# Kernel optimization log

Measured on AMD Instinct MI355X. Metric: run time of the kernel, lower is better.

The kernel has to match this reference:

```python
import jax, jax.numpy as jnp
import numpy as np

B, C, N, M, K = 1, 64, 65536, 65536, 16
H, O = 64, 128  # mlp hidden, out_channels


def setup_inputs() -> dict:
    key = jax.random.key(0)
    ks = jax.random.split(key, 8)
    return {
        "x": jax.random.normal(ks[0], (B, C, N), dtype=jnp.float32),
        "pos": jax.random.normal(ks[1], (B, 3, N), dtype=jnp.float32),
        "support_points": jax.random.normal(ks[2], (B, 3, M), dtype=jnp.float32),
        "W1": jax.random.normal(ks[3], (H, C + 3), dtype=jnp.float32) * 0.05,
        "b1": jax.random.normal(ks[4], (H,), dtype=jnp.float32) * 0.05,
        "W2": jax.random.normal(ks[5], (O, H), dtype=jnp.float32) * 0.05,
        "b2": jax.random.normal(ks[6], (O,), dtype=jnp.float32) * 0.05,
        "indices": jax.random.randint(ks[7], (B, M, K), 0, N, dtype=jnp.int64),
    }


def _gather_points(t, indices):
    # t: [B, C, N], indices: [B, M, K] -> [B, C, M, K]
    b, c, n = t.shape
    m, k = indices.shape[1], indices.shape[2]
    idx = indices.reshape(b, 1, m * k)  # broadcasts over channel dim
    return jnp.take_along_axis(t, idx, axis=2).reshape(b, c, m, k)


def reference(x, pos, support_points, W1, b1, W2, b2, indices):
    # gather neighbor features and positions: [B, C, M, K], [B, 3, M, K]
    feats = _gather_points(x, indices)
    pts = _gather_points(pos, indices) - support_points[:, :, :, None]
    h = jnp.concatenate([feats, pts], axis=1)  # [B, C+3, M, K]
    # shared per-point MLP (1x1 Conv2d == channel contraction)
    h = jnp.einsum("oc,bcmk->bomk", W1, h) + b1[None, :, None, None]
    h = jax.nn.relu(h)
    h = jnp.einsum("oc,bcmk->bomk", W2, h) + b2[None, :, None, None]
    # max-pool over neighborhood K -> [B, O, M]
    return jnp.max(h, axis=3)
```

## Files before the change

### kernel.cpp

```cpp
#include <hip/hip_runtime.h>

#define NPTS 65536
#define MPTS 65536
#define FSTR 88

typedef __attribute__((ext_vector_type(8))) short bf16x8;
typedef __attribute__((ext_vector_type(4))) float f32x4;

__device__ __forceinline__ float bflo(unsigned int u){ union{unsigned int i; float f;} v; v.i = u<<16; return v.f; }
__device__ __forceinline__ float bfhi(unsigned int u){ union{unsigned int i; float f;} v; v.i = u & 0xffff0000u; return v.f; }
__device__ __forceinline__ unsigned short f2bf(float f){
  union{float f; unsigned int i;} v; v.f=f;
  unsigned int r = v.i + 0x7fffu + ((v.i>>16)&1u);
  return (unsigned short)(r>>16);
}

__global__ __launch_bounds__(256) void pack_all(
    const float* __restrict__ x, const float* __restrict__ pos,
    const float* __restrict__ W1, const float* __restrict__ W2,
    unsigned short* __restrict__ P2,
    unsigned short* __restrict__ W1F, unsigned short* __restrict__ W2F) {
  __shared__ unsigned int tile[64 * 37];
  const int t = threadIdx.x;
  const int n0 = blockIdx.x * 64;
  const int p = t & 63, cq = t >> 6;
  const int n = n0 + p;
  #pragma unroll
  for (int jj = 0; jj < 8; ++jj) {
    const int c = cq * 16 + 2 * jj;
    const unsigned int lo = f2bf(x[(size_t)c * NPTS + n]);
    const unsigned int hi = f2bf(x[(size_t)(c + 1) * NPTS + n]);
    tile[p * 37 + cq * 8 + jj] = lo | (hi << 16);
  }
  if (cq == 0) {
    const unsigned int a = f2bf(pos[n]);
    const unsigned int b = f2bf(pos[NPTS + n]);
    const unsigned int cc = f2bf(pos[2 * NPTS + n]);
    tile[p * 37 + 32] = a | (b << 16);
    tile[p * 37 + 33] = cc;
    tile[p * 37 + 34] = 0u;
    tile[p * 37 + 35] = 0u;
  }
  __syncthreads();
  unsigned int* Pd = (unsigned int*)(P2 + (size_t)n0 * 72);
  #pragma unroll
  for (int i = 0; i < 9; ++i) {
    const int u = t + i * 256;
    const int nl = u / 36, d = u - nl * 36;
    Pd[u] = tile[nl * 37 + d];
  }
  if (blockIdx.x < 7) {
    const int f = blockIdx.x * 256 + t;
    if (f < 768) {
      const int kt = f >> 8, rem = f & 255, nt = rem >> 6, lane = rem & 63;
      const int h = nt*16 + (lane & 15);
      const int c0 = kt*32 + (lane >> 4) * 8;
      #pragma unroll
      for (int j = 0; j < 8; ++j) {
        const int c = c0 + j;
        W1F[f*8 + j] = (c < 67) ? f2bf(W1[h*67 + c]) : (unsigned short)0;
      }
    } else if (f < 1792) {
      const int g = f - 768;
      const int kt = g >> 9, rem = g & 511, ot = rem >> 6, lane = rem & 63;
      const int o = ot*16 + (lane & 15);
      const int h0 = kt*32 + (lane >> 4) * 8;
      #pragma unroll
      for (int j = 0; j < 8; ++j) W2F[g*8 + j] = f2bf(W2[o*64 + h0 + j]);
    }
  }
}

#define MFMA16(a,b,c) __builtin_amdgcn_mfma_f32_16x16x32_bf16((a),(b),(c),0,0,0)

__global__ __launch_bounds__(256, 3) void pointnet_mfma(
    const unsigned short* __restrict__ P2,
    const float* __restrict__ sup,
    const unsigned short* __restrict__ W1F,
    const float* __restrict__ b1,
    const unsigned short* __restrict__ W2F,
    const float* __restrict__ b2,
    const int* __restrict__ indices,
    float* __restrict__ out) {
  __shared__ __align__(16) char smem[53248];
  unsigned short* featB = (unsigned short*)smem;
  unsigned short* hlds  = (unsigned short*)smem;
  float* smax = (float*)(smem + 45056);

  const int t = threadIdx.x;
  const int m0 = blockIdx.x * 16;
  const int lane = t & 63, w = t >> 6, quad = lane >> 4, lr = lane & 15;

  {
    const int idx = indices[m0*16 + t];
    const uint4* src = (const uint4*)(P2 + (size_t)idx * 72);
    uint4 u[9];
    #pragma unroll
    for (int i = 0; i < 9; ++i) u[i] = src[i];
    const int mm = m0 + (t >> 4);
    const float s0 = sup[mm], s1 = sup[MPTS + mm], s2 = sup[2*MPTS + mm];
    const float p0 = bflo(u[8].x), p1 = bfhi(u[8].x), p2 = bflo(u[8].y);
    u[8].x = (unsigned int)f2bf(p0 - s0) | ((unsigned int)f2bf(p1 - s1) << 16);
    u[8].y = (unsigned int)f2bf(p2 - s2);
    u[8].z = 0u; u[8].w = 0u;
    uint4* dst = (uint4*)(featB + t * FSTR);
    #pragma unroll
    for (int i = 0; i < 9; ++i) dst[i] = u[i];
  }

  bf16x8 w1f[3][4];
  #pragma unroll
  for (int kt = 0; kt < 3; ++kt)
    #pragma unroll
    for (int nt = 0; nt < 4; ++nt)
      w1f[kt][nt] = ((const bf16x8*)W1F)[(kt*4 + nt)*64 + lane];
  float b1s[4];
  #pragma unroll
  for (int nt = 0; nt < 4; ++nt) b1s[nt] = b1[nt*16 + lr];

  const f32x4 fz = {0.f, 0.f, 0.f, 0.f};
  f32x4 acc[4][4];
  #pragma unroll
  for (int pt = 0; pt < 4; ++pt)
    #pragma unroll
    for (int nt = 0; nt < 4; ++nt) acc[pt][nt] = fz;
  #pragma unroll
  for (int kt = 0; kt < 2; ++kt) {
    bf16x8 af[4];
    #pragma unroll
    for (int pt = 0; pt < 4; ++pt)
      af[pt] = *(const bf16x8*)&featB[(w*64 + pt*16 + lr)*FSTR + kt*32 + quad*8];
    #pragma unroll
    for (int pt = 0; pt < 4; ++pt)
      #pragma unroll
      for (int nt = 0; nt < 4; ++nt)
        acc[pt][nt] = MFMA16(af[pt], w1f[kt][nt], acc[pt][nt]);
  }
  {
    const bf16x8 zv = {0,0,0,0,0,0,0,0};
    bf16x8 af[4];
    #pragma unroll
    for (int pt = 0; pt < 4; ++pt) {
      const bf16x8 v = *(const bf16x8*)&featB[(w*64 + pt*16 + lr)*FSTR + 64];
      af[pt] = (quad == 0) ? v : zv;
    }
    #pragma unroll
    for (int pt = 0; pt < 4; ++pt)
      #pragma unroll
      for (int nt = 0; nt < 4; ++nt)
        acc[pt][nt] = MFMA16(af[pt], w1f[2][nt], acc[pt][nt]);
  }

  #pragma unroll
  for (int pt = 0; pt < 4; ++pt)
    #pragma unroll
    for (int nt = 0; nt < 4; ++nt) {
      const int h = nt*16 + lr;
      const int pbase = w*64 + pt*16 + quad*4;
      #pragma unroll
      for (int r = 0; r < 4; ++r)
        hlds[(pbase + r)*FSTR + h] = f2bf(fmaxf(acc[pt][nt][r] + b1s[nt], 0.f));
    }

  #pragma unroll
  for (int oh = 0; oh < 2; ++oh) {
    bf16x8 w2f[2][4];
    #pragma unroll
    for (int kt = 0; kt < 2; ++kt)
      #pragma unroll
      for (int ot = 0; ot < 4; ++ot)
        w2f[kt][ot] = ((const bf16x8*)W2F)[(kt*8 + oh*4 + ot)*64 + lane];
    f32x4 a2[4][4];
    #pragma unroll
    for (int pt = 0; pt < 4; ++pt)
      #pragma unroll
      for (int ot = 0; ot < 4; ++ot) a2[pt][ot] = fz;
    #pragma unroll
    for (int kt = 0; kt < 2; ++kt) {
      bf16x8 ah[4];
      #pragma unroll
      for (int pt = 0; pt < 4; ++pt)
        ah[pt] = *(const bf16x8*)&hlds[(w*64 + pt*16 + lr)*FSTR + kt*32 + quad*8];
      #pragma unroll
      for (int pt = 0; pt < 4; ++pt)
        #pragma unroll
        for (int ot = 0; ot < 4; ++ot)
          a2[pt][ot] = MFMA16(ah[pt], w2f[kt][ot], a2[pt][ot]);
    }
    #pragma unroll
    for (int pt = 0; pt < 4; ++pt)
      #pragma unroll
      for (int ot = 0; ot < 4; ++ot) {
        f32x4 v4 = a2[pt][ot];
        float v = fmaxf(fmaxf(v4[0], v4[1]), fmaxf(v4[2], v4[3]));
        v = fmaxf(v, __shfl_xor(v, 16));
        v = fmaxf(v, __shfl_xor(v, 32));
        if (quad == 0) smax[(w*4 + pt)*128 + oh*64 + ot*16 + lr] = v;
      }
  }
  __syncthreads();

  #pragma unroll
  for (int i = 0; i < 2; ++i) {
    const int u = t + i*256;
    const int o = u >> 2, mg = u & 3;
    const float bb = b2[o];
    float4 val;
    val.x = smax[(mg*4 + 0)*128 + o] + bb;
    val.y = smax[(mg*4 + 1)*128 + o] + bb;
    val.z = smax[(mg*4 + 2)*128 + o] + bb;
    val.w = smax[(mg*4 + 3)*128 + o] + bb;
    *(float4*)(out + (size_t)o * MPTS + m0 + mg*4) = val;
  }
}

__global__ __launch_bounds__(256) void pointnet_fallback(
    const float* __restrict__ x, const float* __restrict__ pos,
    const float* __restrict__ sup,
    const float* __restrict__ W1, const float* __restrict__ b1,
    const float* __restrict__ W2, const float* __restrict__ b2,
    const int* __restrict__ indices, float* __restrict__ out) {
  __shared__ float sfeat[16][68];
  __shared__ float shid[16][64];
  __shared__ float smax[4][128];
  __shared__ int sidx[16];
  const int t = threadIdx.x;
  const int m = blockIdx.x;
  if (t < 16) sidx[t] = indices[m*16 + t];
  const float sup0 = sup[m], sup1 = sup[MPTS + m], sup2 = sup[2*MPTS + m];
  __syncthreads();
  for (int u = t; u < 16*17; u += 256) {
    const int k = u / 17, c4 = (u - k*17) * 4;
    const int idx = sidx[k];
    float4 w;
    if (c4 < 64) {
      w.x = x[(size_t)(c4+0)*NPTS + idx]; w.y = x[(size_t)(c4+1)*NPTS + idx];
      w.z = x[(size_t)(c4+2)*NPTS + idx]; w.w = x[(size_t)(c4+3)*NPTS + idx];
    } else {
      w.x = pos[idx] - sup0; w.y = pos[NPTS + idx] - sup1;
      w.z = pos[2*NPTS + idx] - sup2; w.w = 0.f;
    }
    *(float4*)&sfeat[k][c4] = w;
  }
  const int h = t & 63, kg = t >> 6;
  float w1r[68];
  #pragma unroll
  for (int c = 0; c < 67; ++c) w1r[c] = W1[h*67 + c];
  w1r[67] = 0.f;
  const float bias1 = b1[h];
  __syncthreads();
  #pragma unroll
  for (int j = 0; j < 4; ++j) {
    const int k = kg*4 + j;
    float a = bias1;
    const float4* rr = (const float4*)sfeat[k];
    #pragma unroll
    for (int q = 0; q < 17; ++q) {
      const float4 v = rr[q];
      a += w1r[q*4+0]*v.x + w1r[q*4+1]*v.y + w1r[q*4+2]*v.z + w1r[q*4+3]*v.w;
    }
    shid[k][h] = fmaxf(a, 0.f);
  }
  const int ow = t & 63;
  float w2a[64], w2b[64];
  #pragma unroll
  for (int hh = 0; hh < 64; ++hh) { w2a[hh] = W2[ow*64 + hh]; w2b[hh] = W2[(ow+64)*64 + hh]; }
  __syncthreads();
  float mxa = -3.0e38f, mxb = -3.0e38f;
  #pragma unroll
  for (int j = 0; j < 4; ++j) {
    const int k = kg*4 + j;
    const float4* hr = (const float4*)shid[k];
    float pa = 0.f, pb = 0.f;
    #pragma unroll
    for (int q = 0; q < 16; ++q) {
      const float4 v = hr[q];
      pa += w2a[q*4+0]*v.x + w2a[q*4+1]*v.y + w2a[q*4+2]*v.z + w2a[q*4+3]*v.w;
      pb += w2b[q*4+0]*v.x + w2b[q*4+1]*v.y + w2b[q*4+2]*v.z + w2b[q*4+3]*v.w;
    }
    mxa = fmaxf(mxa, pa); mxb = fmaxf(mxb, pb);
  }
  smax[kg][ow] = mxa; smax[kg][64 + ow] = mxb;
  __syncthreads();
  if (t < 128) {
    out[(size_t)t * MPTS + m] =
        fmaxf(fmaxf(smax[0][t], smax[1][t]), fmaxf(smax[2][t], smax[3][t])) + b2[t];
  }
}

extern "C" void kernel_launch(void* const* d_in, const int* in_sizes, int n_in,
                              void* d_out, int out_size, void* d_ws, size_t ws_size,
                              hipStream_t stream) {
  const float* x   = (const float*)d_in[0];
  const float* pos = (const float*)d_in[1];
  const float* sup = (const float*)d_in[2];
  const float* W1  = (const float*)d_in[3];
  const float* b1  = (const float*)d_in[4];
  const float* W2  = (const float*)d_in[5];
  const float* b2  = (const float*)d_in[6];
  const int* indices = (const int*)d_in[7];
  float* out = (float*)d_out;

  const size_t P2_BYTES  = (size_t)NPTS * 72 * 2;
  const size_t W1F_BYTES = 768 * 8 * 2;
  const size_t W2F_BYTES = 1024 * 8 * 2;
  if (ws_size >= P2_BYTES + W1F_BYTES + W2F_BYTES) {
    unsigned short* P2  = (unsigned short*)d_ws;
    unsigned short* W1F = (unsigned short*)((char*)d_ws + P2_BYTES);
    unsigned short* W2F = (unsigned short*)((char*)d_ws + P2_BYTES + W1F_BYTES);
    pack_all<<<NPTS/64, 256, 0, stream>>>(x, pos, W1, W2, P2, W1F, W2F);
    pointnet_mfma<<<MPTS/16, 256, 0, stream>>>(P2, sup, W1F, b1, W2F, b2, indices, out);
  } else {
    pointnet_fallback<<<MPTS, 256, 0, stream>>>(x, pos, sup, W1, b1, W2, b2, indices, out);
  }
}
```

Before: 153.3 us.

## Keep hidden layer in registers via transposed MFMA, drop LDS round-trip and smax

```diff
diff --git a/kernel.cpp b/kernel.cpp
--- a/kernel.cpp
+++ b/kernel.cpp
@@ -2,7 +2,7 @@
 
 #define NPTS 65536
 #define MPTS 65536
-#define FSTR 88
+#define FSTR 72
 
 typedef __attribute__((ext_vector_type(8))) short bf16x8;
 typedef __attribute__((ext_vector_type(4))) float f32x4;
@@ -15,11 +15,14 @@
   return (unsigned short)(r>>16);
 }
 
+#define MFMA32(a,b,c) __builtin_amdgcn_mfma_f32_16x16x32_bf16((a),(b),(c),0,0,0)
+
 __global__ __launch_bounds__(256) void pack_all(
     const float* __restrict__ x, const float* __restrict__ pos,
     const float* __restrict__ W1, const float* __restrict__ W2,
     unsigned short* __restrict__ P2,
-    unsigned short* __restrict__ W1F, unsigned short* __restrict__ W2F) {
+    unsigned short* __restrict__ W1F,
+    unsigned short* __restrict__ W2F) {
   __shared__ unsigned int tile[64 * 37];
   const int t = threadIdx.x;
   const int n0 = blockIdx.x * 64;
@@ -42,38 +45,42 @@
     tile[p * 37 + 35] = 0u;
   }
   __syncthreads();
-  unsigned int* Pd = (unsigned int*)(P2 + (size_t)n0 * 72);
+  unsigned int* Pd = (unsigned int*)(P2 + (size_t)n0 * FSTR);
   #pragma unroll
   for (int i = 0; i < 9; ++i) {
     const int u = t + i * 256;
     const int nl = u / 36, d = u - nl * 36;
     Pd[u] = tile[nl * 37 + d];
   }
-  if (blockIdx.x < 7) {
-    const int f = blockIdx.x * 256 + t;
-    if (f < 768) {
-      const int kt = f >> 8, rem = f & 255, nt = rem >> 6, lane = rem & 63;
-      const int h = nt*16 + (lane & 15);
-      const int c0 = kt*32 + (lane >> 4) * 8;
+  const int wid = blockIdx.x * 256 + t;
+  if (wid < 768) {
+    const int f = wid >> 6, lane = wid & 63;
+    const int q = lane >> 4, lr = lane & 15;
+    if (f < 8) {
+      const int kt = f >> 2, nt = f & 3;
+      #pragma unroll
+      for (int j = 0; j < 8; ++j)
+        W1F[wid*8 + j] = f2bf(W1[(nt*16 + lr)*67 + kt*32 + q*8 + j]);
+    } else {
+      const int nt = f - 8;
       #pragma unroll
       for (int j = 0; j < 8; ++j) {
-        const int c = c0 + j;
-        W1F[f*8 + j] = (c < 67) ? f2bf(W1[h*67 + c]) : (unsigned short)0;
+        const int c = 64 + q*4 + j;
+        W1F[wid*8 + j] = (j < 4 && c < 67) ? f2bf(W1[(nt*16 + lr)*67 + c]) : (unsigned short)0;
       }
-    } else if (f < 1792) {
-      const int g = f - 768;
-      const int kt = g >> 9, rem = g & 511, ot = rem >> 6, lane = rem & 63;
-      const int o = ot*16 + (lane & 15);
-      const int h0 = kt*32 + (lane >> 4) * 8;
-      #pragma unroll
-      for (int j = 0; j < 8; ++j) W2F[g*8 + j] = f2bf(W2[o*64 + h0 + j]);
-    }
-  }
-}
-
-#define MFMA16(a,b,c) __builtin_amdgcn_mfma_f32_16x16x32_bf16((a),(b),(c),0,0,0)
-
-__global__ __launch_bounds__(256, 3) void pointnet_mfma(
+    }
+  } else if (wid < 768 + 2048) {
+    const int gg = wid - 768;
+    const int g = gg >> 6, lane = gg & 63;
+    const int q = lane >> 4, lr = lane & 15;
+    const int nt = g >> 3, ot = g & 7;
+    #pragma unroll
+    for (int j = 0; j < 8; ++j)
+      W2F[gg*8 + j] = (j < 4) ? f2bf(W2[(ot*16 + lr)*64 + nt*16 + q*4 + j]) : (unsigned short)0;
+  }
+}
+
+__global__ __launch_bounds__(256, 4) void pointnet_mfma(
     const unsigned short* __restrict__ P2,
     const float* __restrict__ sup,
     const unsigned short* __restrict__ W1F,
@@ -82,10 +89,7 @@
     const float* __restrict__ b2,
     const int* __restrict__ indices,
     float* __restrict__ out) {
-  __shared__ __align__(16) char smem[53248];
-  unsigned short* featB = (unsigned short*)smem;
-  unsigned short* hlds  = (unsigned short*)smem;
-  float* smax = (float*)(smem + 45056);
+  __shared__ __align__(16) unsigned short featB[256 * FSTR];
 
   const int t = threadIdx.x;
   const int m0 = blockIdx.x * 16;
@@ -93,7 +97,7 @@
 
   {
     const int idx = indices[m0*16 + t];
-    const uint4* src = (const uint4*)(P2 + (size_t)idx * 72);
+    const uint4* src = (const uint4*)(P2 + (size_t)idx * FSTR);
     uint4 u[9];
     #pragma unroll
     for (int i = 0; i < 9; ++i) u[i] = src[i];
@@ -108,109 +112,92 @@
     for (int i = 0; i < 9; ++i) dst[i] = u[i];
   }
 
-  bf16x8 w1f[3][4];
-  #pragma unroll
-  for (int kt = 0; kt < 3; ++kt)
+  const f32x4 fz = {0.f, 0.f, 0.f, 0.f};
+  f32x4 acc1[4][4];
+  #pragma unroll
+  for (int nt = 0; nt < 4; ++nt)
+    #pragma unroll
+    for (int pt = 0; pt < 4; ++pt) acc1[nt][pt] = fz;
+
+  #pragma unroll
+  for (int kt = 0; kt < 2; ++kt) {
+    bf16x8 wa[4];
     #pragma unroll
     for (int nt = 0; nt < 4; ++nt)
-      w1f[kt][nt] = ((const bf16x8*)W1F)[(kt*4 + nt)*64 + lane];
-  float b1s[4];
-  #pragma unroll
-  for (int nt = 0; nt < 4; ++nt) b1s[nt] = b1[nt*16 + lr];
-
-  const f32x4 fz = {0.f, 0.f, 0.f, 0.f};
-  f32x4 acc[4][4];
-  #pragma unroll
-  for (int pt = 0; pt < 4; ++pt)
-    #pragma unroll
-    for (int nt = 0; nt < 4; ++nt) acc[pt][nt] = fz;
-  #pragma unroll
-  for (int kt = 0; kt < 2; ++kt) {
-    bf16x8 af[4];
+      wa[nt] = ((const bf16x8*)W1F)[(kt*4 + nt)*64 + lane];
+    bf16x8 bf[4];
     #pragma unroll
     for (int pt = 0; pt < 4; ++pt)
-      af[pt] = *(const bf16x8*)&featB[(w*64 + pt*16 + lr)*FSTR + kt*32 + quad*8];
-    #pragma unroll
-    for (int pt = 0; pt < 4; ++pt)
-      #pragma unroll
-      for (int nt = 0; nt < 4; ++nt)
-        acc[pt][nt] = MFMA16(af[pt], w1f[kt][nt], acc[pt][nt]);
+      bf[pt] = *(const bf16x8*)&featB[(w*64 + pt*16 + lr)*FSTR + kt*32 + quad*8];
+    #pragma unroll
+    for (int nt = 0; nt < 4; ++nt)
+      #pragma unroll
+      for (int pt = 0; pt < 4; ++pt)
+        acc1[nt][pt] = MFMA32(wa[nt], bf[pt], acc1[nt][pt]);
   }
   {
-    const bf16x8 zv = {0,0,0,0,0,0,0,0};
-    bf16x8 af[4];
+    bf16x8 wa16[4];
+    #pragma unroll
+    for (int nt = 0; nt < 4; ++nt)
+      wa16[nt] = ((const bf16x8*)W1F)[(8 + nt)*64 + lane];
+    bf16x8 bt[4];
     #pragma unroll
     for (int pt = 0; pt < 4; ++pt) {
-      const bf16x8 v = *(const bf16x8*)&featB[(w*64 + pt*16 + lr)*FSTR + 64];
-      af[pt] = (quad == 0) ? v : zv;
-    }
-    #pragma unroll
-    for (int pt = 0; pt < 4; ++pt)
-      #pragma unroll
-      for (int nt = 0; nt < 4; ++nt)
-        acc[pt][nt] = MFMA16(af[pt], w1f[2][nt], acc[pt][nt]);
-  }
-
-  #pragma unroll
-  for (int pt = 0; pt < 4; ++pt)
+      const uint2 d = *(const uint2*)&featB[(w*64 + pt*16 + lr)*FSTR + 64 + (quad & 1)*4];
+      union { unsigned int u[4]; bf16x8 v; } mk;
+      mk.u[0] = d.x; mk.u[1] = d.y; mk.u[2] = 0u; mk.u[3] = 0u;
+      bt[pt] = mk.v;
+    }
+    #pragma unroll
+    for (int nt = 0; nt < 4; ++nt)
+      #pragma unroll
+      for (int pt = 0; pt < 4; ++pt)
+        acc1[nt][pt] = MFMA32(wa16[nt], bt[pt], acc1[nt][pt]);
+  }
+
+  unsigned int dwpk[4][4][2];
+  #pragma unroll
+  for (int nt = 0; nt < 4; ++nt) {
+    const float4 bb = *(const float4*)(b1 + nt*16 + quad*4);
+    #pragma unroll
+    for (int pt = 0; pt < 4; ++pt) {
+      const float v0 = fmaxf(acc1[nt][pt][0] + bb.x, 0.f);
+      const float v1 = fmaxf(acc1[nt][pt][1] + bb.y, 0.f);
+      const float v2 = fmaxf(acc1[nt][pt][2] + bb.z, 0.f);
+      const float v3 = fmaxf(acc1[nt][pt][3] + bb.w, 0.f);
+      dwpk[nt][pt][0] = (unsigned int)f2bf(v0) | ((unsigned int)f2bf(v1) << 16);
+      dwpk[nt][pt][1] = (unsigned int)f2bf(v2) | ((unsigned int)f2bf(v3) << 16);
+    }
+  }
+
+  #pragma unroll
+  for (int ot = 0; ot < 8; ++ot) {
+    f32x4 a2[4];
+    #pragma unroll
+    for (int pt = 0; pt < 4; ++pt) a2[pt] = fz;
     #pragma unroll
     for (int nt = 0; nt < 4; ++nt) {
-      const int h = nt*16 + lr;
-      const int pbase = w*64 + pt*16 + quad*4;
-      #pragma unroll
-      for (int r = 0; r < 4; ++r)
-        hlds[(pbase + r)*FSTR + h] = f2bf(fmaxf(acc[pt][nt][r] + b1s[nt], 0.f));
-    }
-
-  #pragma unroll
-  for (int oh = 0; oh < 2; ++oh) {
-    bf16x8 w2f[2][4];
-    #pragma unroll
-    for (int kt = 0; kt < 2; ++kt)
-      #pragma unroll
-      for (int ot = 0; ot < 4; ++ot)
-        w2f[kt][ot] = ((const bf16x8*)W2F)[(kt*8 + oh*4 + ot)*64 + lane];
-    f32x4 a2[4][4];
-    #pragma unroll
-    for (int pt = 0; pt < 4; ++pt)
-      #pragma unroll
-      for (int ot = 0; ot < 4; ++ot) a2[pt][ot] = fz;
-    #pragma unroll
-    for (int kt = 0; kt < 2; ++kt) {
-      bf16x8 ah[4];
-      #pragma unroll
-      for (int pt = 0; pt < 4; ++pt)
-        ah[pt] = *(const bf16x8*)&hlds[(w*64 + pt*16 + lr)*FSTR + kt*32 + quad*8];
-      #pragma unroll
-      for (int pt = 0; pt < 4; ++pt)
-        #pragma unroll
-        for (int ot = 0; ot < 4; ++ot)
-          a2[pt][ot] = MFMA16(ah[pt], w2f[kt][ot], a2[pt][ot]);
-    }
-    #pragma unroll
-    for (int pt = 0; pt < 4; ++pt)
-      #pragma unroll
-      for (int ot = 0; ot < 4; ++ot) {
-        f32x4 v4 = a2[pt][ot];
-        float v = fmaxf(fmaxf(v4[0], v4[1]), fmaxf(v4[2], v4[3]));
-        v = fmaxf(v, __shfl_xor(v, 16));
-        v = fmaxf(v, __shfl_xor(v, 32));
-        if (quad == 0) smax[(w*4 + pt)*128 + oh*64 + ot*16 + lr] = v;
+      const bf16x8 wb = ((const bf16x8*)W2F)[(nt*8 + ot)*64 + lane];
+      #pragma unroll
+      for (int pt = 0; pt < 4; ++pt) {
+        union { unsigned int u[4]; bf16x8 v; } mk;
+        mk.u[0] = dwpk[nt][pt][0]; mk.u[1] = dwpk[nt][pt][1];
+        mk.u[2] = 0u; mk.u[3] = 0u;
+        a2[pt] = MFMA32(mk.v, wb, a2[pt]);
       }
-  }
-  __syncthreads();
-
-  #pragma unroll
-  for (int i = 0; i < 2; ++i) {
-    const int u = t + i*256;
-    const int o = u >> 2, mg = u & 3;
-    const float bb = b2[o];
-    float4 val;
-    val.x = smax[(mg*4 + 0)*128 + o] + bb;
-    val.y = smax[(mg*4 + 1)*128 + o] + bb;
-    val.z = smax[(mg*4 + 2)*128 + o] + bb;
-    val.w = smax[(mg*4 + 3)*128 + o] + bb;
-    *(float4*)(out + (size_t)o * MPTS + m0 + mg*4) = val;
+    }
+    float vm[4];
+    #pragma unroll
+    for (int pt = 0; pt < 4; ++pt) {
+      float v = fmaxf(fmaxf(a2[pt][0], a2[pt][1]), fmaxf(a2[pt][2], a2[pt][3]));
+      v = fmaxf(v, __shfl_xor(v, 16));
+      v = fmaxf(v, __shfl_xor(v, 32));
+      vm[pt] = v;
+    }
+    const float vq = (quad & 1) ? ((quad & 2) ? vm[3] : vm[1])
+                                : ((quad & 2) ? vm[2] : vm[0]);
+    const int o = ot*16 + lr;
+    out[(size_t)o * MPTS + m0 + w*4 + quad] = vq + b2[o];
   }
 }
 
@@ -232,15 +219,15 @@
   for (int u = t; u < 16*17; u += 256) {
     const int k = u / 17, c4 = (u - k*17) * 4;
     const int idx = sidx[k];
-    float4 w;
+    float4 wv;
     if (c4 < 64) {
-      w.x = x[(size_t)(c4+0)*NPTS + idx]; w.y = x[(size_t)(c4+1)*NPTS + idx];
-      w.z = x[(size_t)(c4+2)*NPTS + idx]; w.w = x[(size_t)(c4+3)*NPTS + idx];
+      wv.x = x[(size_t)(c4+0)*NPTS + idx]; wv.y = x[(size_t)(c4+1)*NPTS + idx];
+      wv.z = x[(size_t)(c4+2)*NPTS + idx]; wv.w = x[(size_t)(c4+3)*NPTS + idx];
     } else {
-      w.x = pos[idx] - sup0; w.y = pos[NPTS + idx] - sup1;
-      w.z = pos[2*NPTS + idx] - sup2; w.w = 0.f;
-    }
-    *(float4*)&sfeat[k][c4] = w;
+      wv.x = pos[idx] - sup0; wv.y = pos[NPTS + idx] - sup1;
+      wv.z = pos[2*NPTS + idx] - sup2; wv.w = 0.f;
+    }
+    *(float4*)&sfeat[k][c4] = wv;
   }
   const int h = t & 63, kg = t >> 6;
   float w1r[68];
@@ -255,9 +242,9 @@
     float a = bias1;
     const float4* rr = (const float4*)sfeat[k];
     #pragma unroll
-    for (int q = 0; q < 17; ++q) {
-      const float4 v = rr[q];
-      a += w1r[q*4+0]*v.x + w1r[q*4+1]*v.y + w1r[q*4+2]*v.z + w1r[q*4+3]*v.w;
+    for (int qq = 0; qq < 17; ++qq) {
+      const float4 v = rr[qq];
+      a += w1r[qq*4+0]*v.x + w1r[qq*4+1]*v.y + w1r[qq*4+2]*v.z + w1r[qq*4+3]*v.w;
     }
     shid[k][h] = fmaxf(a, 0.f);
   }
@@ -273,10 +260,10 @@
     const float4* hr = (const float4*)shid[k];
     float pa = 0.f, pb = 0.f;
     #pragma unroll
-    for (int q = 0; q < 16; ++q) {
-      const float4 v = hr[q];
-      pa += w2a[q*4+0]*v.x + w2a[q*4+1]*v.y + w2a[q*4+2]*v.z + w2a[q*4+3]*v.w;
-      pb += w2b[q*4+0]*v.x + w2b[q*4+1]*v.y + w2b[q*4+2]*v.z + w2b[q*4+3]*v.w;
+    for (int qq = 0; qq < 16; ++qq) {
+      const float4 v = hr[qq];
+      pa += w2a[qq*4+0]*v.x + w2a[qq*4+1]*v.y + w2a[qq*4+2]*v.z + w2a[qq*4+3]*v.w;
+      pb += w2b[qq*4+0]*v.x + w2b[qq*4+1]*v.y + w2b[qq*4+2]*v.z + w2b[qq*4+3]*v.w;
     }
     mxa = fmaxf(mxa, pa); mxb = fmaxf(mxb, pb);
   }
@@ -301,9 +288,9 @@
   const int* indices = (const int*)d_in[7];
   float* out = (float*)d_out;
 
-  const size_t P2_BYTES  = (size_t)NPTS * 72 * 2;
-  const size_t W1F_BYTES = 768 * 8 * 2;
-  const size_t W2F_BYTES = 1024 * 8 * 2;
+  const size_t P2_BYTES  = (size_t)NPTS * FSTR * 2;
+  const size_t W1F_BYTES = 12 * 64 * 8 * 2;
+  const size_t W2F_BYTES = 32 * 64 * 8 * 2;
   if (ws_size >= P2_BYTES + W1F_BYTES + W2F_BYTES) {
     unsigned short* P2  = (unsigned short*)d_ws;
     unsigned short* W1F = (unsigned short*)((char*)d_ws + P2_BYTES);
```

After: 155.7 us. Within noise of the previous version (+1.6%).
